# Kernel tuning notes

Hardware: AMD Instinct MI355X
Metric: run time of the kernel (lower is better)

Reference implementation:

```python
import jax, jax.numpy as jnp
import numpy as np

B, T, C, H, E = 4, 128, 256, 8, 64  # batch, tokens, n_embd, n_head, edge_dim
D = C // H


def setup_inputs() -> dict:
    key = jax.random.key(0)
    ks = jax.random.split(key, 12)
    s = 0.02
    return {
        "x": jax.random.normal(ks[0], (B, T, C), jnp.float32),
        "aux_x": jax.random.normal(ks[1], (B, T, C), jnp.float32),
        "mask": jnp.ones((B, T, T), jnp.int32),
        "edge": jax.random.normal(ks[2], (B, T, T, E), jnp.float32),
        "Wq": jax.random.normal(ks[3], (C, C), jnp.float32) * s,
        "bq": jnp.zeros((C,), jnp.float32),
        "Wk": jax.random.normal(ks[4], (C, C + E), jnp.float32) * s,
        "bk": jnp.zeros((C,), jnp.float32),
        "Wv": jax.random.normal(ks[5], (C, C + E), jnp.float32) * s,
        "bv": jnp.zeros((C,), jnp.float32),
        "Wp": jax.random.normal(ks[6], (C, C), jnp.float32) * s,
        "bp": jnp.zeros((C,), jnp.float32),
    }


def reference(x, aux_x, mask, edge, Wq, bq, Wk, bk, Wv, bv, Wp, bp):
    Bx, Tx, Cx = x.shape
    q = x @ Wq.T + bq  # [B,T,C]
    # per-pair augmented features: node i broadcast over all j, concat edge(i,j)
    aug = jnp.concatenate(
        [jnp.broadcast_to(x[:, :, None, :], (Bx, Tx, Tx, Cx)), edge], axis=-1
    )  # [B,T,T,C+E]
    k = aug @ Wk.T + bk  # [B,T,T,C]
    v = aug @ Wv.T + bv  # [B,T,T,C]
    q = q.reshape(Bx, Tx, H, D).transpose(0, 2, 1, 3)          # [B,H,T,D]
    k = k.reshape(Bx, Tx, Tx, H, D).transpose(0, 3, 1, 2, 4)   # [B,H,T,T,D]
    v = v.reshape(Bx, Tx, Tx, H, D).transpose(0, 3, 1, 2, 4)   # [B,H,T,T,D]
    att = jnp.einsum('bhid,bhijd->bhij', q, k) * (1.0 / jnp.sqrt(jnp.float32(D)))
    att = jnp.where(mask[:, None] == 0, -jnp.inf, att)
    all_masked = (mask == 0).all(-1)[:, None, :, None]  # rows with no valid key
    att = jnp.where(all_masked, 0.0, att)
    fi = jnp.finfo(att.dtype)
    att = jnp.nan_to_num(att, nan=0.0, posinf=fi.max, neginf=fi.min)
    att = jax.nn.softmax(att, axis=-1)
    y = jnp.einsum('bhij,bhijd->bhid', att, v)  # [B,H,T,D]
    y = y.transpose(0, 2, 1, 3).reshape(Bx, Tx, Cx)
    return y @ Wp.T + bp
```

## Files before the change

kernel.cpp:

```cpp
#include <hip/hip_runtime.h>

#define SENT (-3.402823466e38f)

typedef __attribute__((ext_vector_type(8))) short short8;
typedef __attribute__((ext_vector_type(4))) float floatx4;

#define OFF_QKP   0
#define OFF_AGG   131072
#define OFF_VNODE 262144

__device__ __forceinline__ ushort f2b(float f) {
    uint u = __float_as_uint(f);
    u += 0x7FFFu + ((u >> 16) & 1u);
    return (ushort)(u >> 16);
}
__device__ __forceinline__ short8 pk8(float4 a, float4 b) {
    short8 r;
    r[0]=(short)f2b(a.x); r[1]=(short)f2b(a.y); r[2]=(short)f2b(a.z); r[3]=(short)f2b(a.w);
    r[4]=(short)f2b(b.x); r[5]=(short)f2b(b.y); r[6]=(short)f2b(b.z); r[7]=(short)f2b(b.w);
    return r;
}

__global__ __launch_bounds__(256, 4)
void k1_proj(const float* __restrict__ x, const float* __restrict__ Wq,
             const float* __restrict__ Wv, const float* __restrict__ Wk,
             const float* __restrict__ bq, const float* __restrict__ bv,
             float* __restrict__ vnode, ushort* __restrict__ qkp) {
    __shared__ float xL[16][264];
    __shared__ float qls[16][66];
    int tid = threadIdx.x;
    int w = tid >> 6, lane = tid & 63, g = lane >> 4, r = lane & 15;
    int m  = blockIdx.x & 1;
    int ct = (blockIdx.x >> 1) & 3;
    int rt = blockIdx.x >> 3;
    int r0 = rt*16, c0 = ct*64;

    #pragma unroll
    for (int it = 0; it < 4; ++it) {
        int fid = (tid + 256*it)*4;
        int rr = fid >> 8, k = fid & 255;
        *(float4*)&xL[rr][k] = *(const float4*)&x[(size_t)(r0+rr)*256 + k];
    }
    __syncthreads();

    int c = c0 + w*16 + r;
    const float* Wrow = m ? (Wv + (size_t)c*320) : (Wq + (size_t)c*256);
    floatx4 acc = {0.f,0.f,0.f,0.f};
    #pragma unroll
    for (int kt = 0; kt < 8; ++kt) {
        int k0 = kt*32 + g*8;
        short8 af = pk8(*(float4*)&xL[r][k0], *(float4*)&xL[r][k0+4]);
        short8 bf = pk8(*(const float4*)&Wrow[k0], *(const float4*)&Wrow[k0+4]);
        acc = __builtin_amdgcn_mfma_f32_16x16x32_bf16(af, bf, acc, 0,0,0);
    }
    float bb = m ? bv[c] : bq[c];
    if (m) {
        #pragma unroll
        for (int i = 0; i < 4; ++i)
            vnode[(size_t)(r0 + 4*g + i)*256 + c] = acc[i] + bb;
    } else {
        #pragma unroll
        for (int i = 0; i < 4; ++i)
            qls[4*g + i][w*16 + r] = acc[i] + bb;
        __syncthreads();
        int rr = tid >> 4, es = tid & 15;
        int h0 = ct*2;
        float a0[4] = {0,0,0,0}, a1[4] = {0,0,0,0};
        const float* wk0 = Wk + (size_t)(h0*32)*320 + 256 + es*4;
        const float* wk1 = Wk + (size_t)((h0+1)*32)*320 + 256 + es*4;
        #pragma unroll 8
        for (int d = 0; d < 32; ++d) {
            float q0 = qls[rr][d];
            float q1 = qls[rr][32 + d];
            float4 w0 = *(const float4*)&wk0[(size_t)d*320];
            float4 w1 = *(const float4*)&wk1[(size_t)d*320];
            a0[0]+=q0*w0.x; a0[1]+=q0*w0.y; a0[2]+=q0*w0.z; a0[3]+=q0*w0.w;
            a1[0]+=q1*w1.x; a1[1]+=q1*w1.y; a1[2]+=q1*w1.z; a1[3]+=q1*w1.w;
        }
        const float s = 0.17677669529663687f;
        ushort4 u0, u1;
        u0.x=f2b(a0[0]*s); u0.y=f2b(a0[1]*s); u0.z=f2b(a0[2]*s); u0.w=f2b(a0[3]*s);
        u1.x=f2b(a1[0]*s); u1.y=f2b(a1[1]*s); u1.z=f2b(a1[2]*s); u1.w=f2b(a1[3]*s);
        size_t base = (size_t)(r0 + rr)*512;
        *(ushort4*)&qkp[base + h0*64 + es*4]     = u0;
        *(ushort4*)&qkp[base + (h0+1)*64 + es*4] = u1;
    }
}

__global__ __launch_bounds__(256, 4)
void k2_attn(const float* __restrict__ edge, const int* __restrict__ msk,
             const ushort* __restrict__ qkp, ushort* __restrict__ aggO) {
    __shared__ ushort edsA[128][72];
    __shared__ ushort qkpL[16][64];
    __shared__ float  attL[8][132];
    __shared__ ushort attT[16][136];
    __shared__ float  mval[128];
    int tid = threadIdx.x;
    int w = tid >> 6, lane = tid & 63, g = lane >> 4, r = lane & 15;
    int row = blockIdx.x;

    float4 ef[8];
    const float* eg = edge + (size_t)row*8192;
    #pragma unroll
    for (int it = 0; it < 8; ++it)
        ef[it] = *(const float4*)(eg + (size_t)(tid + 256*it)*4);

    {
        ushort* qf = (ushort*)qkpL;
        *(uint*)&qf[tid*2]       = *(const uint*)&qkp[(size_t)row*512 + tid*2];
        *(uint*)&qf[512 + tid*2] = 0u;
    }
    if (tid < 128) mval[tid] = (msk[(size_t)row*128 + tid] != 0) ? 1.0f : 0.0f;
    if (tid < 136) {
        #pragma unroll
        for (int hp = 8; hp < 16; ++hp) attT[hp][tid] = 0;
    }
    #pragma unroll
    for (int it = 0; it < 8; ++it) {
        int fid = (tid + 256*it)*4;
        int j = fid >> 6, e = fid & 63;
        uint lo = (uint)f2b(ef[it].x) | ((uint)f2b(ef[it].y) << 16);
        uint hi = (uint)f2b(ef[it].z) | ((uint)f2b(ef[it].w) << 16);
        *(uint2*)&edsA[j][e] = make_uint2(lo, hi);
    }
    __syncthreads();

    {
        #pragma unroll
        for (int mi = 0; mi < 2; ++mi) {
            int mt = w*2 + mi;
            floatx4 acc = {0,0,0,0};
            #pragma unroll
            for (int kt = 0; kt < 2; ++kt) {
                short8 af = *(short8*)&edsA[mt*16 + r][kt*32 + g*8];
                short8 bf = *(short8*)&qkpL[r][kt*32 + g*8];
                acc = __builtin_amdgcn_mfma_f32_16x16x32_bf16(af, bf, acc, 0,0,0);
            }
            if (r < 8) {
                #pragma unroll
                for (int i = 0; i < 4; ++i) {
                    int j = mt*16 + 4*g + i;
                    attL[r][j] = (mval[j] > 0.5f) ? acc[i] : SENT;
                }
            }
        }
    }
    __syncthreads();

    {
        #pragma unroll
        for (int hh = 0; hh < 2; ++hh) {
            int h = w*2 + hh;
            float v0 = attL[h][lane];
            float v1 = attL[h][64 + lane];
            float mx = fmaxf(v0, v1);
            #pragma unroll
            for (int off = 32; off >= 1; off >>= 1) mx = fmaxf(mx, __shfl_xor(mx, off));
            float e0 = __expf(v0 - mx), e1 = __expf(v1 - mx);
            float sm = e0 + e1;
            #pragma unroll
            for (int off = 32; off >= 1; off >>= 1) sm += __shfl_xor(sm, off);
            float inv = 1.0f / sm;
            attT[h][lane]      = f2b(e0 * inv);
            attT[h][64 + lane] = f2b(e1 * inv);
        }
    }
    __syncthreads();

    {
        floatx4 acc = {0,0,0,0};
        #pragma unroll
        for (int kt = 0; kt < 4; ++kt) {
            short8 a2 = *(short8*)&attT[r][kt*32 + g*8];
            short8 b2;
            #pragma unroll
            for (int jj = 0; jj < 8; ++jj)
                b2[jj] = (short)edsA[kt*32 + g*8 + jj][w*16 + r];
            acc = __builtin_amdgcn_mfma_f32_16x16x32_bf16(a2, b2, acc, 0,0,0);
        }
        #pragma unroll
        for (int i = 0; i < 4; ++i) {
            int h = 4*g + i;
            if (h < 8)
                aggO[(size_t)row*512 + h*64 + w*16 + r] = f2b(acc[i]);
        }
    }
}

__global__ __launch_bounds__(256, 2)
void k3_out(const float* __restrict__ vnode, const ushort* __restrict__ aggI,
            const float* __restrict__ Wv, const float* __restrict__ Wp,
            const float* __restrict__ bp, float* __restrict__ out) {
    __shared__ ushort yL[16][264];
    int tid = threadIdx.x;
    int w = tid >> 6, lane = tid & 63, g = lane >> 4, r = lane & 15;
    int rt = blockIdx.x >> 2, ob = blockIdx.x & 3;
    int r0 = rt*16, o0 = ob*64;

    {
        #pragma unroll
        for (int pi = 0; pi < 4; ++pi) {
            int p = w*4 + pi, h = p >> 1, ntl = p & 1;
            int c = h*32 + ntl*16 + r;
            floatx4 acc;
            #pragma unroll
            for (int i = 0; i < 4; ++i)
                acc[i] = vnode[(size_t)(r0 + 4*g + i)*256 + c];
            #pragma unroll
            for (int kt = 0; kt < 2; ++kt) {
                short8 af = *(const short8*)&aggI[(size_t)(r0 + r)*512 + h*64 + kt*32 + g*8];
                const float* wr = Wv + (size_t)c*320 + 256 + kt*32 + g*8;
                short8 bf = pk8(*(const float4*)wr, *(const float4*)(wr + 4));
                acc = __builtin_amdgcn_mfma_f32_16x16x32_bf16(af, bf, acc, 0,0,0);
            }
            #pragma unroll
            for (int i = 0; i < 4; ++i)
                yL[4*g + i][c] = f2b(acc[i]);
        }
    }
    __syncthreads();

    {
        int o = o0 + w*16 + r;
        floatx4 acc = {0,0,0,0};
        const float* wr = Wp + (size_t)o*256;
        #pragma unroll
        for (int kt = 0; kt < 8; ++kt) {
            int k0 = kt*32 + g*8;
            short8 af = *(short8*)&yL[r][k0];
            short8 bf = pk8(*(const float4*)&wr[k0], *(const float4*)&wr[k0+4]);
            acc = __builtin_amdgcn_mfma_f32_16x16x32_bf16(af, bf, acc, 0,0,0);
        }
        float bb = bp[o];
        #pragma unroll
        for (int i = 0; i < 4; ++i)
            out[(size_t)(r0 + 4*g + i)*256 + o] = acc[i] + bb;
    }
}

extern "C" void kernel_launch(void* const* d_in, const int* in_sizes, int n_in,
                              void* d_out, int out_size, void* d_ws, size_t ws_size,
                              hipStream_t stream) {
    (void)in_sizes; (void)n_in; (void)out_size; (void)ws_size;
    const float* x    = (const float*)d_in[0];
    const int*   msk  = (const int*)d_in[2];
    const float* edge = (const float*)d_in[3];
    const float* Wq   = (const float*)d_in[4];
    const float* bq   = (const float*)d_in[5];
    const float* Wk   = (const float*)d_in[6];
    const float* Wv   = (const float*)d_in[8];
    const float* bv   = (const float*)d_in[9];
    const float* Wp   = (const float*)d_in[10];
    const float* bp   = (const float*)d_in[11];
    float* out = (float*)d_out;
    float* ws  = (float*)d_ws;

    ushort* qkp   = (ushort*)(ws + OFF_QKP);
    ushort* agg   = (ushort*)(ws + OFF_AGG);
    float*  vnode = ws + OFF_VNODE;

    k1_proj<<<256, 256, 0, stream>>>(x, Wq, Wv, Wk, bq, bv, vnode, qkp);
    k2_attn<<<512, 256, 0, stream>>>(edge, msk, qkp, agg);
    k3_out<<<128, 256, 0, stream>>>(vnode, agg, Wv, Wp, bp, out);
}
```

Measured before the change: 21.49 us.

## Split K across warps and raise block counts in all three kernels

k1 now uses 512 blocks of 32 columns, splits the K dimension across warp pairs and reduces the partials through shared memory, with each q block computing one head's edge projection. k2 goes to 512 threads, so each wave handles one key tile and one head's softmax. k3 uses 512 blocks of 16 output columns with a split-K reduction. The aim is more parallelism and fewer serial MFMA chains per wave on a small problem. The cost is extra shared-memory reductions and barriers, and k3 redundantly recomputes the y tile in 4x more blocks.

```diff
diff --git a/kernel.cpp b/kernel.cpp
--- a/kernel.cpp
+++ b/kernel.cpp
@@ -22,18 +22,19 @@
 }
 
 __global__ __launch_bounds__(256, 4)
-void k1_proj(const float* __restrict__ x, const float* __restrict__ Wq,
-             const float* __restrict__ Wv, const float* __restrict__ Wk,
-             const float* __restrict__ bq, const float* __restrict__ bv,
+void k1_proj(const float* __restrict__ x,
+             const float* __restrict__ Wq, const float* __restrict__ bq,
+             const float* __restrict__ Wk, const float* __restrict__ Wv,
+             const float* __restrict__ bv,
              float* __restrict__ vnode, ushort* __restrict__ qkp) {
     __shared__ float xL[16][264];
-    __shared__ float qls[16][66];
+    __shared__ float red[4][64][4];
+    __shared__ float qls[16][34];
     int tid = threadIdx.x;
     int w = tid >> 6, lane = tid & 63, g = lane >> 4, r = lane & 15;
-    int m  = blockIdx.x & 1;
-    int ct = (blockIdx.x >> 1) & 3;
-    int rt = blockIdx.x >> 3;
-    int r0 = rt*16, c0 = ct*64;
+    int b = blockIdx.x;
+    int rt = b >> 4, ct = (b >> 1) & 7, m = b & 1;
+    int r0 = rt*16, c0 = ct*32, h = ct;
 
     #pragma unroll
     for (int it = 0; it < 4; ++it) {
@@ -43,51 +44,52 @@
     }
     __syncthreads();
 
-    int c = c0 + w*16 + r;
+    int nt = w & 1, ks = w >> 1;
+    int c = c0 + nt*16 + r;
     const float* Wrow = m ? (Wv + (size_t)c*320) : (Wq + (size_t)c*256);
     floatx4 acc = {0.f,0.f,0.f,0.f};
     #pragma unroll
-    for (int kt = 0; kt < 8; ++kt) {
+    for (int kt = ks*4; kt < ks*4+4; ++kt) {
         int k0 = kt*32 + g*8;
         short8 af = pk8(*(float4*)&xL[r][k0], *(float4*)&xL[r][k0+4]);
         short8 bf = pk8(*(const float4*)&Wrow[k0], *(const float4*)&Wrow[k0+4]);
         acc = __builtin_amdgcn_mfma_f32_16x16x32_bf16(af, bf, acc, 0,0,0);
     }
-    float bb = m ? bv[c] : bq[c];
-    if (m) {
-        #pragma unroll
-        for (int i = 0; i < 4; ++i)
-            vnode[(size_t)(r0 + 4*g + i)*256 + c] = acc[i] + bb;
-    } else {
-        #pragma unroll
-        for (int i = 0; i < 4; ++i)
-            qls[4*g + i][w*16 + r] = acc[i] + bb;
-        __syncthreads();
-        int rr = tid >> 4, es = tid & 15;
-        int h0 = ct*2;
-        float a0[4] = {0,0,0,0}, a1[4] = {0,0,0,0};
-        const float* wk0 = Wk + (size_t)(h0*32)*320 + 256 + es*4;
-        const float* wk1 = Wk + (size_t)((h0+1)*32)*320 + 256 + es*4;
+    *(floatx4*)&red[w][lane][0] = acc;
+    __syncthreads();
+
+    {
+        int nt2 = tid >> 7, half = (tid >> 6) & 1, l = tid & 63;
+        int g2 = l >> 4, r2 = l & 15;
+        int c2 = c0 + nt2*16 + r2;
+        #pragma unroll
+        for (int ii = 0; ii < 2; ++ii) {
+            int i = half*2 + ii;
+            float v = red[nt2][l][i] + red[2+nt2][l][i];
+            int row = 4*g2 + i;
+            if (m == 0) qls[row][nt2*16 + r2] = v + bq[c2];
+            else vnode[(size_t)(r0 + row)*256 + c2] = v + bv[c2];
+        }
+    }
+    __syncthreads();
+
+    if (m == 0) {
+        int rr = tid >> 4, e4 = (tid & 15)*4;
+        const float* wk = Wk + (size_t)(h*32)*320 + 256 + e4;
+        float a0=0.f, a1=0.f, a2=0.f, a3=0.f;
         #pragma unroll 8
         for (int d = 0; d < 32; ++d) {
-            float q0 = qls[rr][d];
-            float q1 = qls[rr][32 + d];
-            float4 w0 = *(const float4*)&wk0[(size_t)d*320];
-            float4 w1 = *(const float4*)&wk1[(size_t)d*320];
-            a0[0]+=q0*w0.x; a0[1]+=q0*w0.y; a0[2]+=q0*w0.z; a0[3]+=q0*w0.w;
-            a1[0]+=q1*w1.x; a1[1]+=q1*w1.y; a1[2]+=q1*w1.z; a1[3]+=q1*w1.w;
+            float qd = qls[rr][d];
+            float4 w4 = *(const float4*)&wk[(size_t)d*320];
+            a0 += qd*w4.x; a1 += qd*w4.y; a2 += qd*w4.z; a3 += qd*w4.w;
         }
         const float s = 0.17677669529663687f;
-        ushort4 u0, u1;
-        u0.x=f2b(a0[0]*s); u0.y=f2b(a0[1]*s); u0.z=f2b(a0[2]*s); u0.w=f2b(a0[3]*s);
-        u1.x=f2b(a1[0]*s); u1.y=f2b(a1[1]*s); u1.z=f2b(a1[2]*s); u1.w=f2b(a1[3]*s);
-        size_t base = (size_t)(r0 + rr)*512;
-        *(ushort4*)&qkp[base + h0*64 + es*4]     = u0;
-        *(ushort4*)&qkp[base + (h0+1)*64 + es*4] = u1;
-    }
-}
-
-__global__ __launch_bounds__(256, 4)
+        ushort4 u; u.x=f2b(a0*s); u.y=f2b(a1*s); u.z=f2b(a2*s); u.w=f2b(a3*s);
+        *(ushort4*)&qkp[(size_t)(r0+rr)*512 + h*64 + e4] = u;
+    }
+}
+
+__global__ __launch_bounds__(512, 4)
 void k2_attn(const float* __restrict__ edge, const int* __restrict__ msk,
              const ushort* __restrict__ qkp, ushort* __restrict__ aggO) {
     __shared__ ushort edsA[128][72];
@@ -99,16 +101,16 @@
     int w = tid >> 6, lane = tid & 63, g = lane >> 4, r = lane & 15;
     int row = blockIdx.x;
 
-    float4 ef[8];
+    float4 ef[4];
     const float* eg = edge + (size_t)row*8192;
     #pragma unroll
-    for (int it = 0; it < 8; ++it)
-        ef[it] = *(const float4*)(eg + (size_t)(tid + 256*it)*4);
-
-    {
+    for (int it = 0; it < 4; ++it)
+        ef[it] = *(const float4*)(eg + (size_t)(tid + 512*it)*4);
+
+    if (tid < 256) {
         ushort* qf = (ushort*)qkpL;
-        *(uint*)&qf[tid*2]       = *(const uint*)&qkp[(size_t)row*512 + tid*2];
-        *(uint*)&qf[512 + tid*2] = 0u;
+        *(uint*)&qf[tid*2]        = *(const uint*)&qkp[(size_t)row*512 + tid*2];
+        *(uint*)&qf[512 + tid*2]  = 0u;
     }
     if (tid < 128) mval[tid] = (msk[(size_t)row*128 + tid] != 0) ? 1.0f : 0.0f;
     if (tid < 136) {
@@ -116,8 +118,8 @@
         for (int hp = 8; hp < 16; ++hp) attT[hp][tid] = 0;
     }
     #pragma unroll
-    for (int it = 0; it < 8; ++it) {
-        int fid = (tid + 256*it)*4;
+    for (int it = 0; it < 4; ++it) {
+        int fid = (tid + 512*it)*4;
         int j = fid >> 6, e = fid & 63;
         uint lo = (uint)f2b(ef[it].x) | ((uint)f2b(ef[it].y) << 16);
         uint hi = (uint)f2b(ef[it].z) | ((uint)f2b(ef[it].w) << 16);
@@ -126,48 +128,42 @@
     __syncthreads();
 
     {
-        #pragma unroll
-        for (int mi = 0; mi < 2; ++mi) {
-            int mt = w*2 + mi;
-            floatx4 acc = {0,0,0,0};
+        int mt = w;
+        floatx4 acc = {0,0,0,0};
+        #pragma unroll
+        for (int kt = 0; kt < 2; ++kt) {
+            short8 af = *(short8*)&edsA[mt*16 + r][kt*32 + g*8];
+            short8 bf = *(short8*)&qkpL[r][kt*32 + g*8];
+            acc = __builtin_amdgcn_mfma_f32_16x16x32_bf16(af, bf, acc, 0,0,0);
+        }
+        if (r < 8) {
             #pragma unroll
-            for (int kt = 0; kt < 2; ++kt) {
-                short8 af = *(short8*)&edsA[mt*16 + r][kt*32 + g*8];
-                short8 bf = *(short8*)&qkpL[r][kt*32 + g*8];
-                acc = __builtin_amdgcn_mfma_f32_16x16x32_bf16(af, bf, acc, 0,0,0);
+            for (int i = 0; i < 4; ++i) {
+                int j = mt*16 + 4*g + i;
+                attL[r][j] = (mval[j] > 0.5f) ? acc[i] : SENT;
             }
-            if (r < 8) {
-                #pragma unroll
-                for (int i = 0; i < 4; ++i) {
-                    int j = mt*16 + 4*g + i;
-                    attL[r][j] = (mval[j] > 0.5f) ? acc[i] : SENT;
-                }
-            }
-        }
-    }
-    __syncthreads();
-
-    {
-        #pragma unroll
-        for (int hh = 0; hh < 2; ++hh) {
-            int h = w*2 + hh;
-            float v0 = attL[h][lane];
-            float v1 = attL[h][64 + lane];
-            float mx = fmaxf(v0, v1);
-            #pragma unroll
-            for (int off = 32; off >= 1; off >>= 1) mx = fmaxf(mx, __shfl_xor(mx, off));
-            float e0 = __expf(v0 - mx), e1 = __expf(v1 - mx);
-            float sm = e0 + e1;
-            #pragma unroll
-            for (int off = 32; off >= 1; off >>= 1) sm += __shfl_xor(sm, off);
-            float inv = 1.0f / sm;
-            attT[h][lane]      = f2b(e0 * inv);
-            attT[h][64 + lane] = f2b(e1 * inv);
-        }
-    }
-    __syncthreads();
-
-    {
+        }
+    }
+    __syncthreads();
+
+    {
+        int h = w;
+        float v0 = attL[h][lane];
+        float v1 = attL[h][64 + lane];
+        float mx = fmaxf(v0, v1);
+        #pragma unroll
+        for (int off = 32; off >= 1; off >>= 1) mx = fmaxf(mx, __shfl_xor(mx, off));
+        float e0 = __expf(v0 - mx), e1 = __expf(v1 - mx);
+        float smv = e0 + e1;
+        #pragma unroll
+        for (int off = 32; off >= 1; off >>= 1) smv += __shfl_xor(smv, off);
+        float inv = 1.0f / smv;
+        attT[h][lane]      = f2b(e0 * inv);
+        attT[h][64 + lane] = f2b(e1 * inv);
+    }
+    __syncthreads();
+
+    if (w < 4) {
         floatx4 acc = {0,0,0,0};
         #pragma unroll
         for (int kt = 0; kt < 4; ++kt) {
@@ -187,54 +183,60 @@
     }
 }
 
-__global__ __launch_bounds__(256, 2)
-void k3_out(const float* __restrict__ vnode, const ushort* __restrict__ aggI,
+__global__ __launch_bounds__(256, 4)
+void k3_out(const float* __restrict__ vnode, const ushort* __restrict__ agg,
             const float* __restrict__ Wv, const float* __restrict__ Wp,
             const float* __restrict__ bp, float* __restrict__ out) {
     __shared__ ushort yL[16][264];
+    __shared__ float red2[4][64][4];
     int tid = threadIdx.x;
     int w = tid >> 6, lane = tid & 63, g = lane >> 4, r = lane & 15;
-    int rt = blockIdx.x >> 2, ob = blockIdx.x & 3;
-    int r0 = rt*16, o0 = ob*64;
-
-    {
-        #pragma unroll
-        for (int pi = 0; pi < 4; ++pi) {
-            int p = w*4 + pi, h = p >> 1, ntl = p & 1;
-            int c = h*32 + ntl*16 + r;
-            floatx4 acc;
-            #pragma unroll
-            for (int i = 0; i < 4; ++i)
-                acc[i] = vnode[(size_t)(r0 + 4*g + i)*256 + c];
-            #pragma unroll
-            for (int kt = 0; kt < 2; ++kt) {
-                short8 af = *(const short8*)&aggI[(size_t)(r0 + r)*512 + h*64 + kt*32 + g*8];
-                const float* wr = Wv + (size_t)c*320 + 256 + kt*32 + g*8;
-                short8 bf = pk8(*(const float4*)wr, *(const float4*)(wr + 4));
-                acc = __builtin_amdgcn_mfma_f32_16x16x32_bf16(af, bf, acc, 0,0,0);
-            }
-            #pragma unroll
-            for (int i = 0; i < 4; ++i)
-                yL[4*g + i][c] = f2b(acc[i]);
-        }
-    }
-    __syncthreads();
-
-    {
-        int o = o0 + w*16 + r;
+    int b = blockIdx.x;
+    int rt = b >> 4, ob = b & 15;
+    int r0 = rt*16, o0 = ob*16;
+
+    #pragma unroll
+    for (int pi = 0; pi < 4; ++pi) {
+        int p = w*4 + pi, h = p >> 1, ntl = p & 1;
+        int c = h*32 + ntl*16 + r;
+        floatx4 acc;
+        #pragma unroll
+        for (int i = 0; i < 4; ++i)
+            acc[i] = vnode[(size_t)(r0 + 4*g + i)*256 + c];
+        #pragma unroll
+        for (int kt = 0; kt < 2; ++kt) {
+            short8 af = *(const short8*)&agg[(size_t)(r0 + r)*512 + h*64 + kt*32 + g*8];
+            const float* wr = Wv + (size_t)c*320 + 256 + kt*32 + g*8;
+            short8 bf = pk8(*(const float4*)wr, *(const float4*)(wr + 4));
+            acc = __builtin_amdgcn_mfma_f32_16x16x32_bf16(af, bf, acc, 0,0,0);
+        }
+        #pragma unroll
+        for (int i = 0; i < 4; ++i)
+            yL[4*g + i][c] = f2b(acc[i]);
+    }
+    __syncthreads();
+
+    {
+        int o = o0 + r;
+        const float* wr = Wp + (size_t)o*256;
         floatx4 acc = {0,0,0,0};
-        const float* wr = Wp + (size_t)o*256;
-        #pragma unroll
-        for (int kt = 0; kt < 8; ++kt) {
+        #pragma unroll
+        for (int kt = w*2; kt < w*2+2; ++kt) {
             int k0 = kt*32 + g*8;
             short8 af = *(short8*)&yL[r][k0];
             short8 bf = pk8(*(const float4*)&wr[k0], *(const float4*)&wr[k0+4]);
             acc = __builtin_amdgcn_mfma_f32_16x16x32_bf16(af, bf, acc, 0,0,0);
         }
-        float bb = bp[o];
-        #pragma unroll
-        for (int i = 0; i < 4; ++i)
-            out[(size_t)(r0 + 4*g + i)*256 + o] = acc[i] + bb;
+        *(floatx4*)&red2[w][lane][0] = acc;
+    }
+    __syncthreads();
+
+    {
+        int l = tid >> 2, i = tid & 3;
+        float v = red2[0][l][i] + red2[1][l][i] + red2[2][l][i] + red2[3][l][i];
+        int o = o0 + (l & 15);
+        int row = r0 + 4*(l >> 4) + i;
+        out[(size_t)row*256 + o] = v + bp[o];
     }
 }
 
@@ -259,7 +261,7 @@
     ushort* agg   = (ushort*)(ws + OFF_AGG);
     float*  vnode = ws + OFF_VNODE;
 
-    k1_proj<<<256, 256, 0, stream>>>(x, Wq, Wv, Wk, bq, bv, vnode, qkp);
-    k2_attn<<<512, 256, 0, stream>>>(edge, msk, qkp, agg);
-    k3_out<<<128, 256, 0, stream>>>(vnode, agg, Wv, Wp, bp, out);
-}
+    k1_proj<<<512, 256, 0, stream>>>(x, Wq, bq, Wk, Wv, bv, vnode, qkp);
+    k2_attn<<<512, 512, 0, stream>>>(edge, msk, qkp, agg);
+    k3_out<<<512, 256, 0, stream>>>(vnode, agg, Wv, Wp, bp, out);
+}
```

Result: slower. 24.12 us (+12.2%).
